# Kernel optimization log

Hardware: AMD Instinct MI355X
Metric: run time of the kernel (lower is better)

Reference implementation:

```python
import jax, jax.numpy as jnp
import numpy as np

N_QUBITS = 8
DEPTH = 2
INPUT_DIM = 128
HIDDEN = 128
SEQ = 128
BATCH = 512
DIM = 2 ** N_QUBITS

# Z expectation signs: wire 0 is the most-significant qubit of the state index.
_bits = (np.arange(DIM)[None, :] >> (N_QUBITS - 1 - np.arange(N_QUBITS)[:, None])) & 1
Z_SIGNS = jnp.asarray(1.0 - 2.0 * _bits, dtype=jnp.float32)  # [n_wires, DIM]


def _apply_1q(state, mat, wire):
    """Apply a 2x2 gate on `wire`. mat: [2,2] or batched [bsz,2,2]."""
    bsz = state.shape[0]
    st = state.reshape(bsz, 2 ** wire, 2, -1)
    if mat.ndim == 3:
        out = jnp.einsum('bij,bxjy->bxiy', mat, st)
    else:
        out = jnp.einsum('ij,bxjy->bxiy', mat, st)
    return out.reshape(bsz, DIM)


def _rx_mat(theta):  # theta: [bsz] -> [bsz,2,2] complex
    c = jnp.cos(theta * 0.5).astype(jnp.complex64)
    s = ((-1j) * jnp.sin(theta * 0.5)).astype(jnp.complex64)
    return jnp.stack([jnp.stack([c, s], -1), jnp.stack([s, c], -1)], -2)


def _ry_mat(theta):  # scalar theta -> [2,2] complex
    c = jnp.cos(theta * 0.5)
    s = jnp.sin(theta * 0.5)
    return jnp.stack([jnp.stack([c, -s]), jnp.stack([s, c])]).astype(jnp.complex64)


def _cnot_adj(state, wire):
    """CNOT control=wire, target=wire+1 (adjacent wires)."""
    bsz = state.shape[0]
    st = state.reshape(bsz, 2 ** wire, 4, -1)
    st = st[:, :, jnp.array([0, 1, 3, 2]), :]  # |10>-><|11| swap
    return st.reshape(bsz, DIM)


def _qgate(q_in, params):
    """Variational circuit: RX encoding (first N_QUBITS features of q_in),
    DEPTH x (RY layer + CNOT chain), measure Z on each wire."""
    bsz = q_in.shape[0]
    state = jnp.zeros((bsz, DIM), jnp.complex64).at[:, 0].set(1.0)
    for w in range(N_QUBITS):
        state = _apply_1q(state, _rx_mat(q_in[:, w]), w)
    for d in range(DEPTH):
        for w in range(N_QUBITS):
            state = _apply_1q(state, _ry_mat(params[d, w]), w)
        for w in range(N_QUBITS - 1):
            state = _cnot_adj(state, w)
    probs = state.real ** 2 + state.imag ** 2  # [bsz, DIM]
    return probs @ Z_SIGNS.T  # [bsz, n_wires]


def setup_inputs() -> dict:
    key = jax.random.key(0)
    ks = jax.random.split(key, 16)
    d_in = INPUT_DIM + HIDDEN
    inv = 1.0 / jnp.sqrt(jnp.float32(d_in))
    invq = 1.0 / jnp.sqrt(jnp.float32(N_QUBITS))
    return {
        'inputs': jax.random.normal(ks[0], (SEQ, BATCH, INPUT_DIM), jnp.float32),
        'Wq': jax.random.normal(ks[1], (4 * N_QUBITS, d_in), jnp.float32) * inv,
        'bq': jnp.zeros((4 * N_QUBITS,), jnp.float32),
        'pf': jax.random.normal(ks[2], (DEPTH, N_QUBITS), jnp.float32),
        'pi': jax.random.normal(ks[3], (DEPTH, N_QUBITS), jnp.float32),
        'pg': jax.random.normal(ks[4], (DEPTH, N_QUBITS), jnp.float32),
        'po': jax.random.normal(ks[5], (DEPTH, N_QUBITS), jnp.float32),
        'Wf': jax.random.normal(ks[6], (HIDDEN, N_QUBITS), jnp.float32) * invq,
        'bf': jnp.zeros((HIDDEN,), jnp.float32),
        'Wi': jax.random.normal(ks[7], (HIDDEN, N_QUBITS), jnp.float32) * invq,
        'bi': jnp.zeros((HIDDEN,), jnp.float32),
        'Wg': jax.random.normal(ks[8], (HIDDEN, N_QUBITS), jnp.float32) * invq,
        'bg': jnp.zeros((HIDDEN,), jnp.float32),
        'Wo': jax.random.normal(ks[9], (HIDDEN, N_QUBITS), jnp.float32) * invq,
        'bo': jnp.zeros((HIDDEN,), jnp.float32),
    }


def reference(inputs, Wq, bq, pf, pi, pg, po, Wf, bf, Wi, bi, Wg, bg, Wo, bo):
    bsz = inputs.shape[1]
    h0 = jnp.zeros((bsz, HIDDEN), jnp.float32)
    c0 = jnp.zeros((bsz, HIDDEN), jnp.float32)

    def step(carry, x):
        hx, cx = carry
        combined = jnp.concatenate([x, hx], axis=1)
        q_in = combined @ Wq.T + bq  # [bsz, 4*n_qubits]; only first n_qubits used per gate
        f = jax.nn.sigmoid(_qgate(q_in, pf) @ Wf.T + bf)
        i = jax.nn.sigmoid(_qgate(q_in, pi) @ Wi.T + bi)
        g = jnp.tanh(_qgate(q_in, pg) @ Wg.T + bg)
        o = jax.nn.sigmoid(_qgate(q_in, po) @ Wo.T + bo)
        cx_new = f * cx + i * g
        hx_new = o * jnp.tanh(cx_new)
        return (hx_new, cx_new), hx_new

    (hx, cx), outputs = jax.lax.scan(step, (h0, c0), inputs)
    return outputs, hx, cx
```

## Files before the change

### kernel.cpp

```cpp
#include <hip/hip_runtime.h>

#define SEQ 128
#define BATCH 512
#define IN_DIM 128
#define HID 128

typedef float vf2 __attribute__((ext_vector_type(2)));

#define LOG2E 1.4426950408889634f
#define INV2PI 0.15915494309189535f

__device__ __forceinline__ float rcp_f(float x) { return __builtin_amdgcn_rcpf(x); }
__device__ __forceinline__ float exp2_f(float x) { float r; asm("v_exp_f32 %0, %1" : "=v"(r) : "v"(x)); return r; }
__device__ __forceinline__ float sin2pi_f(float x) { float r; asm("v_sin_f32 %0, %1" : "=v"(r) : "v"(x)); return r; }
__device__ __forceinline__ float cos2pi_f(float x) { float r; asm("v_cos_f32 %0, %1" : "=v"(r) : "v"(x)); return r; }
__device__ __forceinline__ float tanh_f(float x) {
  return 1.0f - 2.0f * rcp_f(exp2_f(x * 2.885390082f) + 1.0f);
}

template <int CTRL>
__device__ __forceinline__ float dpp_add(float s) {
  return s + __int_as_float(__builtin_amdgcn_mov_dpp(__float_as_int(s), CTRL, 0xF, 0xF, true));
}
__device__ __forceinline__ float rdlane(float v, int src) {
  return __int_as_float(__builtin_amdgcn_readlane(__float_as_int(v), src));
}

__global__ __launch_bounds__(64) void qlstm_kernel(
    const float* __restrict__ X, const float* __restrict__ Wq, const float* __restrict__ bq,
    const float* __restrict__ pf, const float* __restrict__ pi_, const float* __restrict__ pg,
    const float* __restrict__ po, const float* __restrict__ Wf, const float* __restrict__ bf,
    const float* __restrict__ Wi, const float* __restrict__ bi, const float* __restrict__ Wg,
    const float* __restrict__ bg, const float* __restrict__ Wo, const float* __restrict__ bo,
    float* __restrict__ out)
{
  __shared__ __align__(16) float h_sh[HID];
  __shared__ __align__(16) float gsh[4 * HID];

  const int lane = threadIdx.x;
  const int r = lane >> 3, c = lane & 7;
  const int g = lane >> 4, p = lane & 15;
  const int b = blockIdx.x;

  const float* gW = (g == 0) ? Wf : (g == 1) ? Wi : (g == 2) ? Wg : Wo;
  const float* gB = (g == 0) ? bf : (g == 1) ? bi : (g == 2) ? bg : bo;
  const float* gP = (g == 0) ? pf : (g == 1) ? pi_ : (g == 2) ? pg : po;

  vf2 wx[8], wh[8];
  {
    const vf2* pxw = (const vf2*)(Wq + r * 256 + 16 * c);
    const vf2* phw = (const vf2*)(Wq + r * 256 + 128 + 16 * c);
#pragma unroll
    for (int j = 0; j < 8; ++j) { wx[j] = pxw[j]; wh[j] = phw[j]; }
  }
  const float bqv = bq[r];

  const float amul = (g == 2) ? 2.0f : 1.0f;
  const float oadd = (g == 2) ? -1.0f : 0.0f;
  const float ksc  = -amul * LOG2E;

  vf2 wg2[8][4];
#pragma unroll
  for (int w = 0; w < 8; ++w)
#pragma unroll
    for (int j = 0; j < 4; ++j) {
      wg2[w][j].x = gW[(8 * p + 2 * j)     * 8 + w] * ksc;
      wg2[w][j].y = gW[(8 * p + 2 * j + 1) * 8 + w] * ksc;
    }
  vf2 bias2[4];
#pragma unroll
  for (int j = 0; j < 4; ++j) {
    bias2[j].x = gB[8 * p + 2 * j]     * ksc;
    bias2[j].y = gB[8 * p + 2 * j + 1] * ksc;
  }
  vf2 cbsb[8]; float C1[8], S1[8];
#pragma unroll
  for (int w = 0; w < 8; ++w) {
    float th0 = gP[w], th1 = gP[8 + w];
    cbsb[w].x = cosf(th0); cbsb[w].y = sinf(th0);
    C1[w] = cosf(th1); S1[w] = sinf(th1);
  }

  vf2 c2; c2.x = 0.f; c2.y = 0.f;
  vf2 h2v; h2v.x = 0.f; h2v.y = 0.f;
  float4 hh0 = {0,0,0,0}, hh1 = {0,0,0,0}, hh2 = {0,0,0,0}, hh3 = {0,0,0,0};

  const float* xg = X + (size_t)b * IN_DIM + 16 * c;
  float* outp = out + (size_t)b * HID + 2 * lane;
  const float4* hp4 = (const float4*)(h_sh + 16 * c);

  float4 xP0, xP1, xP2, xP3, xQ0, xQ1, xQ2, xQ3;
  float xp_cur;
  {
    const float4* x0_ = (const float4*)xg;
    xP0 = x0_[0]; xP1 = x0_[1]; xP2 = x0_[2]; xP3 = x0_[3];
    vf2 ax = wx[0] * (vf2){xP0.x, xP0.y} + wx[1] * (vf2){xP0.z, xP0.w}
           + wx[2] * (vf2){xP1.x, xP1.y} + wx[3] * (vf2){xP1.z, xP1.w}
           + wx[4] * (vf2){xP2.x, xP2.y} + wx[5] * (vf2){xP2.z, xP2.w}
           + wx[6] * (vf2){xP3.x, xP3.y} + wx[7] * (vf2){xP3.z, xP3.w};
    xp_cur = ax.x + ax.y;
    const float4* x1_ = (const float4*)(xg + (size_t)(BATCH * IN_DIM));
    xQ0 = x1_[0]; xQ1 = x1_[1]; xQ2 = x1_[2]; xQ3 = x1_[3];
  }

#define QSTEP(U0, U1, U2, U3, L0, L1, L2, L3, T)                                      \
  {                                                                                   \
                      \
    vf2 aq = (vf2){xp_cur, 0.0f}                                                      \
           + wh[0] * (vf2){hh0.x, hh0.y} + wh[1] * (vf2){hh0.z, hh0.w}                \
           + wh[2] * (vf2){hh1.x, hh1.y} + wh[3] * (vf2){hh1.z, hh1.w}                \
           + wh[4] * (vf2){hh2.x, hh2.y} + wh[5] * (vf2){hh2.z, hh2.w}                \
           + wh[6] * (vf2){hh3.x, hh3.y} + wh[7] * (vf2){hh3.z, hh3.w};               \
    float s_ = aq.x + aq.y;                                                           \
    s_ = dpp_add<0xB1>(s_); s_ = dpp_add<0x4E>(s_); s_ = dpp_add<0x141>(s_);          \
    float z_ = s_ + bqv;                                                              \
    float m_ = z_ * INV2PI;                                                           \
    float sz_ = sin2pi_f(m_), cz_ = cos2pi_f(m_);                                     \
    float cqs[8], sqs[8];                                                             \
    _Pragma("unroll")                                                                 \
    for (int w = 0; w < 8; ++w) { cqs[w] = rdlane(cz_, 8 * w); sqs[w] = rdlane(sz_, 8 * w); } \
                                            \
    vf2 acc0 = bias2[0], acc1 = bias2[1], acc2 = bias2[2], acc3 = bias2[3];           \
    float u_, d_, P_, R_;                                                             \
    {                                                                                 \
      vf2 KA0 = cbsb[0] * cqs[0];                                                     \
      u_ = C1[0]; d_ = C1[0] * KA0.x;                                                 \
      P_ = -S1[0] * KA0.y; R_ = -S1[0] * sqs[0];                                      \
    }                                                                                 \
    _Pragma("unroll")                                                                 \
    for (int w = 1; w < 8; ++w) {                                                     \
      vf2 KA = cbsb[w] * cqs[w];                                                      \
      float K_ = KA.x, A2_ = KA.y, B2_ = sqs[w];                                      \
      float Md = fmaf(A2_, P_, d_);                                                   \
      float MP = fmaf(A2_, d_, P_);                                                   \
      float Mu = fmaf(K_, u_, -(B2_ * R_));                                           \
      float MR = fmaf(B2_, u_, K_ * R_);                                              \
      acc0 += Md * wg2[w - 1][0]; acc1 += Md * wg2[w - 1][1];                         \
      acc2 += Md * wg2[w - 1][2]; acc3 += Md * wg2[w - 1][3];                         \
      u_ = C1[w] * Md; d_ = C1[w] * Mu;                                               \
      P_ = -S1[w] * MP; R_ = -S1[w] * MR;                                             \
    }                                                                                 \
    float ev7_ = d_ + P_;                                                             \
    acc0 += ev7_ * wg2[7][0]; acc1 += ev7_ * wg2[7][1];                               \
    acc2 += ev7_ * wg2[7][2]; acc3 += ev7_ * wg2[7][3];                               \
                     \
    float av_[8] = {acc0.x, acc0.y, acc1.x, acc1.y, acc2.x, acc2.y, acc3.x, acc3.y};  \
    float o8[8];                                                                      \
    _Pragma("unroll")                                                                 \
    for (int k = 0; k < 8; ++k) {                                                     \
      float e_ = exp2_f(av_[k]);                                                      \
      o8[k] = fmaf(rcp_f(1.0f + e_), amul, oadd);                                     \
    }                                                                                 \
    {                                                                                 \
      float4* gp4 = (float4*)(gsh + g * HID + 8 * p);                                 \
      float4 w0; w0.x = o8[0]; w0.y = o8[1]; w0.z = o8[2]; w0.w = o8[3];              \
      float4 w1; w1.x = o8[4]; w1.y = o8[5]; w1.z = o8[6]; w1.w = o8[7];              \
      gp4[0] = w0; gp4[1] = w1;                                                       \
    }                                                                                 \
                          \
    {                                                                                 \
      vf2 axn = wx[0] * (vf2){U0.x, U0.y} + wx[1] * (vf2){U0.z, U0.w}                 \
              + wx[2] * (vf2){U1.x, U1.y} + wx[3] * (vf2){U1.z, U1.w}                 \
              + wx[4] * (vf2){U2.x, U2.y} + wx[5] * (vf2){U2.z, U2.w}                 \
              + wx[6] * (vf2){U3.x, U3.y} + wx[7] * (vf2){U3.z, U3.w};                \
      xp_cur = axn.x + axn.y;                                                         \
      int tl_ = ((T) + 2 < SEQ) ? (T) + 2 : (SEQ - 1);                                \
      const float4* xn_ = (const float4*)(xg + (size_t)tl_ * (BATCH * IN_DIM));       \
      L0 = xn_[0]; L1 = xn_[1]; L2 = xn_[2]; L3 = xn_[3];                             \
    }                                                                                 \
                                   \
    vf2 fv = *(const vf2*)(gsh + 0 * HID + 2 * lane);                                 \
    vf2 iv = *(const vf2*)(gsh + 1 * HID + 2 * lane);                                 \
    vf2 gv = *(const vf2*)(gsh + 2 * HID + 2 * lane);                                 \
    vf2 ov = *(const vf2*)(gsh + 3 * HID + 2 * lane);                                 \
    c2 = fv * c2 + iv * gv;                                                           \
    h2v.x = ov.x * tanh_f(c2.x);                                                      \
    h2v.y = ov.y * tanh_f(c2.y);                                                      \
    *(vf2*)(h_sh + 2 * lane) = h2v;                                                   \
                       \
    hh0 = hp4[0]; hh1 = hp4[1]; hh2 = hp4[2]; hh3 = hp4[3];                           \
    *(vf2*)(outp + (size_t)(T) * (BATCH * HID)) = h2v;                                \
  }

#pragma unroll 1
  for (int tt = 0; tt < SEQ; tt += 2) {
    QSTEP(xQ0, xQ1, xQ2, xQ3, xP0, xP1, xP2, xP3, tt);
    QSTEP(xP0, xP1, xP2, xP3, xQ0, xQ1, xQ2, xQ3, tt + 1);
  }
#undef QSTEP

  {
    size_t base = (size_t)SEQ * BATCH * HID;
    *(vf2*)(out + base + (size_t)b * HID + 2 * lane) = h2v;
    *(vf2*)(out + base + (size_t)BATCH * HID + (size_t)b * HID + 2 * lane) = c2;
  }
}

extern "C" void kernel_launch(void* const* d_in, const int* in_sizes, int n_in,
                              void* d_out, int out_size, void* d_ws, size_t ws_size,
                              hipStream_t stream) {
  (void)in_sizes; (void)n_in; (void)out_size; (void)d_ws; (void)ws_size;
  const float* X   = (const float*)d_in[0];
  const float* Wq  = (const float*)d_in[1];
  const float* bq  = (const float*)d_in[2];
  const float* pf  = (const float*)d_in[3];
  const float* pi_ = (const float*)d_in[4];
  const float* pg  = (const float*)d_in[5];
  const float* po  = (const float*)d_in[6];
  const float* Wf  = (const float*)d_in[7];
  const float* bf  = (const float*)d_in[8];
  const float* Wi  = (const float*)d_in[9];
  const float* bi  = (const float*)d_in[10];
  const float* Wg  = (const float*)d_in[11];
  const float* bg  = (const float*)d_in[12];
  const float* Wo  = (const float*)d_in[13];
  const float* bo  = (const float*)d_in[14];
  float* out = (float*)d_out;

  qlstm_kernel<<<BATCH, 64, 0, stream>>>(X, Wq, bq, pf, pi_, pg, po,
                                         Wf, bf, Wi, bi, Wg, bg, Wo, bo, out);
}
```

Before: 193.1 us.

## Process two batch rows per wavefront to interleave independent recurrent chains

Each 64-lane block now handles two batch elements at once. Their per-step dependency chains are interleaved to expose instruction-level parallelism and hide latency in the serial recurrence. The INV2PI scale is folded into the Wq weights and bias so the per-step multiply goes away. The x prefetch distance changes from two steps to one. The trade-off is half as many blocks (256 instead of 512 on a large GPU) and more registers per thread, which could lower occupancy or leave CUs idle.

```diff
diff --git a/kernel.cpp b/kernel.cpp
--- a/kernel.cpp
+++ b/kernel.cpp
@@ -4,6 +4,7 @@
 #define BATCH 512
 #define IN_DIM 128
 #define HID 128
+#define NCH 2
 
 typedef float vf2 __attribute__((ext_vector_type(2)));
 
@@ -34,13 +35,13 @@
     const float* __restrict__ bg, const float* __restrict__ Wo, const float* __restrict__ bo,
     float* __restrict__ out)
 {
-  __shared__ __align__(16) float h_sh[HID];
-  __shared__ __align__(16) float gsh[4 * HID];
+  __shared__ __align__(16) float gsh[NCH][4 * HID];
+  __shared__ __align__(16) float h_sh[NCH][HID];
 
   const int lane = threadIdx.x;
   const int r = lane >> 3, c = lane & 7;
   const int g = lane >> 4, p = lane & 15;
-  const int b = blockIdx.x;
+  const int b0 = blockIdx.x * NCH;
 
   const float* gW = (g == 0) ? Wf : (g == 1) ? Wi : (g == 2) ? Wg : Wo;
   const float* gB = (g == 0) ? bf : (g == 1) ? bi : (g == 2) ? bg : bo;
@@ -51,9 +52,9 @@
     const vf2* pxw = (const vf2*)(Wq + r * 256 + 16 * c);
     const vf2* phw = (const vf2*)(Wq + r * 256 + 128 + 16 * c);
 #pragma unroll
-    for (int j = 0; j < 8; ++j) { wx[j] = pxw[j]; wh[j] = phw[j]; }
-  }
-  const float bqv = bq[r];
+    for (int j = 0; j < 8; ++j) { wx[j] = pxw[j] * INV2PI; wh[j] = phw[j] * INV2PI; }
+  }
+  const float bqv = bq[r] * INV2PI;
 
   const float amul = (g == 2) ? 2.0f : 1.0f;
   const float oadd = (g == 2) ? -1.0f : 0.0f;
@@ -81,118 +82,151 @@
     C1[w] = cosf(th1); S1[w] = sinf(th1);
   }
 
-  vf2 c2; c2.x = 0.f; c2.y = 0.f;
-  vf2 h2v; h2v.x = 0.f; h2v.y = 0.f;
-  float4 hh0 = {0,0,0,0}, hh1 = {0,0,0,0}, hh2 = {0,0,0,0}, hh3 = {0,0,0,0};
-
-  const float* xg = X + (size_t)b * IN_DIM + 16 * c;
-  float* outp = out + (size_t)b * HID + 2 * lane;
-  const float4* hp4 = (const float4*)(h_sh + 16 * c);
-
-  float4 xP0, xP1, xP2, xP3, xQ0, xQ1, xQ2, xQ3;
-  float xp_cur;
-  {
-    const float4* x0_ = (const float4*)xg;
-    xP0 = x0_[0]; xP1 = x0_[1]; xP2 = x0_[2]; xP3 = x0_[3];
-    vf2 ax = wx[0] * (vf2){xP0.x, xP0.y} + wx[1] * (vf2){xP0.z, xP0.w}
-           + wx[2] * (vf2){xP1.x, xP1.y} + wx[3] * (vf2){xP1.z, xP1.w}
-           + wx[4] * (vf2){xP2.x, xP2.y} + wx[5] * (vf2){xP2.z, xP2.w}
-           + wx[6] * (vf2){xP3.x, xP3.y} + wx[7] * (vf2){xP3.z, xP3.w};
-    xp_cur = ax.x + ax.y;
-    const float4* x1_ = (const float4*)(xg + (size_t)(BATCH * IN_DIM));
-    xQ0 = x1_[0]; xQ1 = x1_[1]; xQ2 = x1_[2]; xQ3 = x1_[3];
-  }
-
-#define QSTEP(U0, U1, U2, U3, L0, L1, L2, L3, T)                                      \
-  {                                                                                   \
-                      \
-    vf2 aq = (vf2){xp_cur, 0.0f}                                                      \
-           + wh[0] * (vf2){hh0.x, hh0.y} + wh[1] * (vf2){hh0.z, hh0.w}                \
-           + wh[2] * (vf2){hh1.x, hh1.y} + wh[3] * (vf2){hh1.z, hh1.w}                \
-           + wh[4] * (vf2){hh2.x, hh2.y} + wh[5] * (vf2){hh2.z, hh2.w}                \
-           + wh[6] * (vf2){hh3.x, hh3.y} + wh[7] * (vf2){hh3.z, hh3.w};               \
-    float s_ = aq.x + aq.y;                                                           \
-    s_ = dpp_add<0xB1>(s_); s_ = dpp_add<0x4E>(s_); s_ = dpp_add<0x141>(s_);          \
-    float z_ = s_ + bqv;                                                              \
-    float m_ = z_ * INV2PI;                                                           \
-    float sz_ = sin2pi_f(m_), cz_ = cos2pi_f(m_);                                     \
-    float cqs[8], sqs[8];                                                             \
-    _Pragma("unroll")                                                                 \
-    for (int w = 0; w < 8; ++w) { cqs[w] = rdlane(cz_, 8 * w); sqs[w] = rdlane(sz_, 8 * w); } \
-                                            \
-    vf2 acc0 = bias2[0], acc1 = bias2[1], acc2 = bias2[2], acc3 = bias2[3];           \
-    float u_, d_, P_, R_;                                                             \
-    {                                                                                 \
-      vf2 KA0 = cbsb[0] * cqs[0];                                                     \
-      u_ = C1[0]; d_ = C1[0] * KA0.x;                                                 \
-      P_ = -S1[0] * KA0.y; R_ = -S1[0] * sqs[0];                                      \
-    }                                                                                 \
-    _Pragma("unroll")                                                                 \
-    for (int w = 1; w < 8; ++w) {                                                     \
-      vf2 KA = cbsb[w] * cqs[w];                                                      \
-      float K_ = KA.x, A2_ = KA.y, B2_ = sqs[w];                                      \
-      float Md = fmaf(A2_, P_, d_);                                                   \
-      float MP = fmaf(A2_, d_, P_);                                                   \
-      float Mu = fmaf(K_, u_, -(B2_ * R_));                                           \
-      float MR = fmaf(B2_, u_, K_ * R_);                                              \
-      acc0 += Md * wg2[w - 1][0]; acc1 += Md * wg2[w - 1][1];                         \
-      acc2 += Md * wg2[w - 1][2]; acc3 += Md * wg2[w - 1][3];                         \
-      u_ = C1[w] * Md; d_ = C1[w] * Mu;                                               \
-      P_ = -S1[w] * MP; R_ = -S1[w] * MR;                                             \
-    }                                                                                 \
-    float ev7_ = d_ + P_;                                                             \
-    acc0 += ev7_ * wg2[7][0]; acc1 += ev7_ * wg2[7][1];                               \
-    acc2 += ev7_ * wg2[7][2]; acc3 += ev7_ * wg2[7][3];                               \
-                     \
-    float av_[8] = {acc0.x, acc0.y, acc1.x, acc1.y, acc2.x, acc2.y, acc3.x, acc3.y};  \
-    float o8[8];                                                                      \
-    _Pragma("unroll")                                                                 \
-    for (int k = 0; k < 8; ++k) {                                                     \
-      float e_ = exp2_f(av_[k]);                                                      \
-      o8[k] = fmaf(rcp_f(1.0f + e_), amul, oadd);                                     \
-    }                                                                                 \
-    {                                                                                 \
-      float4* gp4 = (float4*)(gsh + g * HID + 8 * p);                                 \
-      float4 w0; w0.x = o8[0]; w0.y = o8[1]; w0.z = o8[2]; w0.w = o8[3];              \
-      float4 w1; w1.x = o8[4]; w1.y = o8[5]; w1.z = o8[6]; w1.w = o8[7];              \
-      gp4[0] = w0; gp4[1] = w1;                                                       \
-    }                                                                                 \
-                          \
-    {                                                                                 \
-      vf2 axn = wx[0] * (vf2){U0.x, U0.y} + wx[1] * (vf2){U0.z, U0.w}                 \
-              + wx[2] * (vf2){U1.x, U1.y} + wx[3] * (vf2){U1.z, U1.w}                 \
-              + wx[4] * (vf2){U2.x, U2.y} + wx[5] * (vf2){U2.z, U2.w}                 \
-              + wx[6] * (vf2){U3.x, U3.y} + wx[7] * (vf2){U3.z, U3.w};                \
-      xp_cur = axn.x + axn.y;                                                         \
-      int tl_ = ((T) + 2 < SEQ) ? (T) + 2 : (SEQ - 1);                                \
-      const float4* xn_ = (const float4*)(xg + (size_t)tl_ * (BATCH * IN_DIM));       \
-      L0 = xn_[0]; L1 = xn_[1]; L2 = xn_[2]; L3 = xn_[3];                             \
-    }                                                                                 \
-                                   \
-    vf2 fv = *(const vf2*)(gsh + 0 * HID + 2 * lane);                                 \
-    vf2 iv = *(const vf2*)(gsh + 1 * HID + 2 * lane);                                 \
-    vf2 gv = *(const vf2*)(gsh + 2 * HID + 2 * lane);                                 \
-    vf2 ov = *(const vf2*)(gsh + 3 * HID + 2 * lane);                                 \
-    c2 = fv * c2 + iv * gv;                                                           \
-    h2v.x = ov.x * tanh_f(c2.x);                                                      \
-    h2v.y = ov.y * tanh_f(c2.y);                                                      \
-    *(vf2*)(h_sh + 2 * lane) = h2v;                                                   \
-                       \
-    hh0 = hp4[0]; hh1 = hp4[1]; hh2 = hp4[2]; hh3 = hp4[3];                           \
-    *(vf2*)(outp + (size_t)(T) * (BATCH * HID)) = h2v;                                \
+  vf2 c2[NCH], h2v[NCH];
+  float4 hh[NCH][4];
+  float xp_cur[NCH];
+  const float* xg[NCH];
+  float* outp[NCH];
+#pragma unroll
+  for (int e = 0; e < NCH; ++e) {
+    c2[e].x = 0.f; c2[e].y = 0.f;
+    h2v[e].x = 0.f; h2v[e].y = 0.f;
+#pragma unroll
+    for (int j = 0; j < 4; ++j) { hh[e][j].x = 0.f; hh[e][j].y = 0.f; hh[e][j].z = 0.f; hh[e][j].w = 0.f; }
+    xg[e]   = X   + (size_t)(b0 + e) * IN_DIM + 16 * c;
+    outp[e] = out + (size_t)(b0 + e) * HID + 2 * lane;
+    const float4* x0_ = (const float4*)xg[e];
+    float4 a0 = x0_[0], a1 = x0_[1], a2 = x0_[2], a3 = x0_[3];
+    vf2 ax = wx[0] * (vf2){a0.x, a0.y} + wx[1] * (vf2){a0.z, a0.w}
+           + wx[2] * (vf2){a1.x, a1.y} + wx[3] * (vf2){a1.z, a1.w}
+           + wx[4] * (vf2){a2.x, a2.y} + wx[5] * (vf2){a2.z, a2.w}
+           + wx[6] * (vf2){a3.x, a3.y} + wx[7] * (vf2){a3.z, a3.w};
+    xp_cur[e] = ax.x + ax.y;
   }
 
 #pragma unroll 1
-  for (int tt = 0; tt < SEQ; tt += 2) {
-    QSTEP(xQ0, xQ1, xQ2, xQ3, xP0, xP1, xP2, xP3, tt);
-    QSTEP(xP0, xP1, xP2, xP3, xQ0, xQ1, xQ2, xQ3, tt + 1);
-  }
-#undef QSTEP
+  for (int t = 0; t < SEQ; ++t) {
+    float zz[NCH];
+#pragma unroll
+    for (int e = 0; e < NCH; ++e) {
+      vf2 aq = (vf2){xp_cur[e], 0.0f}
+             + wh[0] * (vf2){hh[e][0].x, hh[e][0].y} + wh[1] * (vf2){hh[e][0].z, hh[e][0].w}
+             + wh[2] * (vf2){hh[e][1].x, hh[e][1].y} + wh[3] * (vf2){hh[e][1].z, hh[e][1].w}
+             + wh[4] * (vf2){hh[e][2].x, hh[e][2].y} + wh[5] * (vf2){hh[e][2].z, hh[e][2].w}
+             + wh[6] * (vf2){hh[e][3].x, hh[e][3].y} + wh[7] * (vf2){hh[e][3].z, hh[e][3].w};
+      float s_ = aq.x + aq.y;
+      s_ = dpp_add<0xB1>(s_); s_ = dpp_add<0x4E>(s_); s_ = dpp_add<0x141>(s_);
+      zz[e] = s_ + bqv;
+    }
+    float szv[NCH], czv[NCH];
+#pragma unroll
+    for (int e = 0; e < NCH; ++e) { szv[e] = sin2pi_f(zz[e]); czv[e] = cos2pi_f(zz[e]); }
+
+    float4 xl[NCH][4];
+    {
+      const int tn = (t + 1 < SEQ) ? t + 1 : SEQ - 1;
+#pragma unroll
+      for (int e = 0; e < NCH; ++e) {
+        const float4* xn_ = (const float4*)(xg[e] + (size_t)tn * (BATCH * IN_DIM));
+#pragma unroll
+        for (int j = 0; j < 4; ++j) xl[e][j] = xn_[j];
+      }
+    }
+
+    float cqs[NCH][8], sqs[NCH][8];
+#pragma unroll
+    for (int e = 0; e < NCH; ++e)
+#pragma unroll
+      for (int w = 0; w < 8; ++w) {
+        cqs[e][w] = rdlane(czv[e], 8 * w);
+        sqs[e][w] = rdlane(szv[e], 8 * w);
+      }
+
+    vf2 acc[NCH][4];
+    float u_[NCH], d_[NCH], P_[NCH], R_[NCH];
+#pragma unroll
+    for (int e = 0; e < NCH; ++e) {
+      acc[e][0] = bias2[0]; acc[e][1] = bias2[1]; acc[e][2] = bias2[2]; acc[e][3] = bias2[3];
+      vf2 KA0 = cbsb[0] * cqs[e][0];
+      u_[e] = C1[0]; d_[e] = C1[0] * KA0.x;
+      P_[e] = -S1[0] * KA0.y; R_[e] = -S1[0] * sqs[e][0];
+    }
+#pragma unroll
+    for (int w = 1; w < 8; ++w) {
+#pragma unroll
+      for (int e = 0; e < NCH; ++e) {
+        vf2 KA = cbsb[w] * cqs[e][w];
+        float K_ = KA.x, A2_ = KA.y, B2_ = sqs[e][w];
+        float Md = fmaf(A2_, P_[e], d_[e]);
+        float MP = fmaf(A2_, d_[e], P_[e]);
+        float Mu = fmaf(K_, u_[e], -(B2_ * R_[e]));
+        float MR = fmaf(B2_, u_[e], K_ * R_[e]);
+        acc[e][0] += Md * wg2[w - 1][0]; acc[e][1] += Md * wg2[w - 1][1];
+        acc[e][2] += Md * wg2[w - 1][2]; acc[e][3] += Md * wg2[w - 1][3];
+        u_[e] = C1[w] * Md; d_[e] = C1[w] * Mu;
+        P_[e] = -S1[w] * MP; R_[e] = -S1[w] * MR;
+      }
+    }
+#pragma unroll
+    for (int e = 0; e < NCH; ++e) {
+      float ev7_ = d_[e] + P_[e];
+      acc[e][0] += ev7_ * wg2[7][0]; acc[e][1] += ev7_ * wg2[7][1];
+      acc[e][2] += ev7_ * wg2[7][2]; acc[e][3] += ev7_ * wg2[7][3];
+    }
+
+#pragma unroll
+    for (int e = 0; e < NCH; ++e) {
+      float av_[8] = {acc[e][0].x, acc[e][0].y, acc[e][1].x, acc[e][1].y,
+                      acc[e][2].x, acc[e][2].y, acc[e][3].x, acc[e][3].y};
+      float o8[8];
+#pragma unroll
+      for (int k = 0; k < 8; ++k) {
+        float ex_ = exp2_f(av_[k]);
+        o8[k] = fmaf(rcp_f(1.0f + ex_), amul, oadd);
+      }
+      float4* gp4 = (float4*)(&gsh[e][g * HID + 8 * p]);
+      float4 w0; w0.x = o8[0]; w0.y = o8[1]; w0.z = o8[2]; w0.w = o8[3];
+      float4 w1; w1.x = o8[4]; w1.y = o8[5]; w1.z = o8[6]; w1.w = o8[7];
+      gp4[0] = w0; gp4[1] = w1;
+    }
+
+#pragma unroll
+    for (int e = 0; e < NCH; ++e) {
+      vf2 fv = *(const vf2*)(&gsh[e][0 * HID + 2 * lane]);
+      vf2 iv = *(const vf2*)(&gsh[e][1 * HID + 2 * lane]);
+      vf2 gv = *(const vf2*)(&gsh[e][2 * HID + 2 * lane]);
+      vf2 ov = *(const vf2*)(&gsh[e][3 * HID + 2 * lane]);
+      c2[e] = fv * c2[e] + iv * gv;
+      h2v[e].x = ov.x * tanh_f(c2[e].x);
+      h2v[e].y = ov.y * tanh_f(c2[e].y);
+      *(vf2*)(&h_sh[e][2 * lane]) = h2v[e];
+    }
+#pragma unroll
+    for (int e = 0; e < NCH; ++e) {
+      const float4* hp4 = (const float4*)(&h_sh[e][16 * c]);
+      hh[e][0] = hp4[0]; hh[e][1] = hp4[1]; hh[e][2] = hp4[2]; hh[e][3] = hp4[3];
+    }
+#pragma unroll
+    for (int e = 0; e < NCH; ++e)
+      *(vf2*)(outp[e] + (size_t)t * (BATCH * HID)) = h2v[e];
+
+#pragma unroll
+    for (int e = 0; e < NCH; ++e) {
+      vf2 axn = wx[0] * (vf2){xl[e][0].x, xl[e][0].y} + wx[1] * (vf2){xl[e][0].z, xl[e][0].w}
+              + wx[2] * (vf2){xl[e][1].x, xl[e][1].y} + wx[3] * (vf2){xl[e][1].z, xl[e][1].w}
+              + wx[4] * (vf2){xl[e][2].x, xl[e][2].y} + wx[5] * (vf2){xl[e][2].z, xl[e][2].w}
+              + wx[6] * (vf2){xl[e][3].x, xl[e][3].y} + wx[7] * (vf2){xl[e][3].z, xl[e][3].w};
+      xp_cur[e] = axn.x + axn.y;
+    }
+  }
 
   {
     size_t base = (size_t)SEQ * BATCH * HID;
-    *(vf2*)(out + base + (size_t)b * HID + 2 * lane) = h2v;
-    *(vf2*)(out + base + (size_t)BATCH * HID + (size_t)b * HID + 2 * lane) = c2;
+#pragma unroll
+    for (int e = 0; e < NCH; ++e) {
+      *(vf2*)(out + base + (size_t)(b0 + e) * HID + 2 * lane) = h2v[e];
+      *(vf2*)(out + base + (size_t)BATCH * HID + (size_t)(b0 + e) * HID + 2 * lane) = c2[e];
+    }
   }
 }
 
@@ -217,6 +251,6 @@
   const float* bo  = (const float*)d_in[14];
   float* out = (float*)d_out;
 
-  qlstm_kernel<<<BATCH, 64, 0, stream>>>(X, Wq, bq, pf, pi_, pg, po,
-                                         Wf, bf, Wi, bi, Wg, bg, Wo, bo, out);
-}
+  qlstm_kernel<<<BATCH / NCH, 64, 0, stream>>>(X, Wq, bq, pf, pi_, pg, po,
+                                               Wf, bf, Wi, bi, Wg, bg, Wo, bo, out);
+}
```

Measured after the change: 217.5 us. 1.13x slower.

## Exchange gate activations via cross-lane permutes instead of LDS round-trip

Applied to the files above, without the earlier changes.

Removes the shared-memory gate buffer. Each lane now gathers its f/i/g/o gate values with permlane32/permlane16 swaps, or a ds_swizzle fallback, followed by selects, and the hidden-unit ownership is remapped so each lane owns units 8p+2g. It also folds the 1/(2π) scale into Wq and bq, balances the dot-product reduction trees, and replaces the two-step unrolled double-buffered x prefetch with a one-step-ahead prefetch. The goal is to cut LDS write/read latency on the serial recurrence critical path, at the cost of more permute and select instructions and a shorter prefetch distance.

```diff
diff --git a/kernel.cpp b/kernel.cpp
--- a/kernel.cpp
+++ b/kernel.cpp
@@ -24,6 +24,25 @@
 }
 __device__ __forceinline__ float rdlane(float v, int src) {
   return __int_as_float(__builtin_amdgcn_readlane(__float_as_int(v), src));
+}
+
+__device__ __forceinline__ void quarter_bcast(float x, float& r0, float& r1, float& r2, float& r3) {
+  unsigned xu = __float_as_uint(x);
+  auto pr = __builtin_amdgcn_permlane32_swap(xu, xu, false, false);
+#if __has_builtin(__builtin_amdgcn_permlane16_swap)
+  auto lo = __builtin_amdgcn_permlane16_swap(pr[0], pr[0], false, false);
+  auto hi = __builtin_amdgcn_permlane16_swap(pr[1], pr[1], false, false);
+  r0 = __uint_as_float(lo[0]); r1 = __uint_as_float(lo[1]);
+  r2 = __uint_as_float(hi[0]); r3 = __uint_as_float(hi[1]);
+#else
+  unsigned s0 = (unsigned)__builtin_amdgcn_ds_swizzle((int)pr[0], 0x401F);
+  unsigned s1 = (unsigned)__builtin_amdgcn_ds_swizzle((int)pr[1], 0x401F);
+  const bool qo = (threadIdx.x >> 4) & 1;
+  r0 = __uint_as_float(qo ? s0 : pr[0]);
+  r1 = __uint_as_float(qo ? pr[0] : s0);
+  r2 = __uint_as_float(qo ? s1 : pr[1]);
+  r3 = __uint_as_float(qo ? pr[1] : s1);
+#endif
 }
 
 __global__ __launch_bounds__(64) void qlstm_kernel(
@@ -35,12 +54,14 @@
     float* __restrict__ out)
 {
   __shared__ __align__(16) float h_sh[HID];
-  __shared__ __align__(16) float gsh[4 * HID];
 
   const int lane = threadIdx.x;
   const int r = lane >> 3, c = lane & 7;
   const int g = lane >> 4, p = lane & 15;
   const int b = blockIdx.x;
+  const int D0 = 8 * p + 2 * g;
+  const bool gsel1 = (g & 1);
+  const bool gsel2 = (g >= 2);
 
   const float* gW = (g == 0) ? Wf : (g == 1) ? Wi : (g == 2) ? Wg : Wo;
   const float* gB = (g == 0) ? bf : (g == 1) ? bi : (g == 2) ? bg : bo;
@@ -51,9 +72,9 @@
     const vf2* pxw = (const vf2*)(Wq + r * 256 + 16 * c);
     const vf2* phw = (const vf2*)(Wq + r * 256 + 128 + 16 * c);
 #pragma unroll
-    for (int j = 0; j < 8; ++j) { wx[j] = pxw[j]; wh[j] = phw[j]; }
-  }
-  const float bqv = bq[r];
+    for (int j = 0; j < 8; ++j) { wx[j] = pxw[j] * INV2PI; wh[j] = phw[j] * INV2PI; }
+  }
+  const float bqv = bq[r] * INV2PI;
 
   const float amul = (g == 2) ? 2.0f : 1.0f;
   const float oadd = (g == 2) ? -1.0f : 0.0f;
@@ -86,113 +107,123 @@
   float4 hh0 = {0,0,0,0}, hh1 = {0,0,0,0}, hh2 = {0,0,0,0}, hh3 = {0,0,0,0};
 
   const float* xg = X + (size_t)b * IN_DIM + 16 * c;
-  float* outp = out + (size_t)b * HID + 2 * lane;
+  float* outp = out + (size_t)b * HID + D0;
   const float4* hp4 = (const float4*)(h_sh + 16 * c);
 
-  float4 xP0, xP1, xP2, xP3, xQ0, xQ1, xQ2, xQ3;
   float xp_cur;
   {
     const float4* x0_ = (const float4*)xg;
-    xP0 = x0_[0]; xP1 = x0_[1]; xP2 = x0_[2]; xP3 = x0_[3];
-    vf2 ax = wx[0] * (vf2){xP0.x, xP0.y} + wx[1] * (vf2){xP0.z, xP0.w}
-           + wx[2] * (vf2){xP1.x, xP1.y} + wx[3] * (vf2){xP1.z, xP1.w}
-           + wx[4] * (vf2){xP2.x, xP2.y} + wx[5] * (vf2){xP2.z, xP2.w}
-           + wx[6] * (vf2){xP3.x, xP3.y} + wx[7] * (vf2){xP3.z, xP3.w};
+    float4 a0 = x0_[0], a1 = x0_[1], a2 = x0_[2], a3 = x0_[3];
+    vf2 t0 = wx[0] * (vf2){a0.x, a0.y} + wx[1] * (vf2){a0.z, a0.w};
+    vf2 t1 = wx[2] * (vf2){a1.x, a1.y} + wx[3] * (vf2){a1.z, a1.w};
+    vf2 t2 = wx[4] * (vf2){a2.x, a2.y} + wx[5] * (vf2){a2.z, a2.w};
+    vf2 t3 = wx[6] * (vf2){a3.x, a3.y} + wx[7] * (vf2){a3.z, a3.w};
+    vf2 ax = (t0 + t1) + (t2 + t3);
     xp_cur = ax.x + ax.y;
-    const float4* x1_ = (const float4*)(xg + (size_t)(BATCH * IN_DIM));
-    xQ0 = x1_[0]; xQ1 = x1_[1]; xQ2 = x1_[2]; xQ3 = x1_[3];
-  }
-
-#define QSTEP(U0, U1, U2, U3, L0, L1, L2, L3, T)                                      \
-  {                                                                                   \
-                      \
-    vf2 aq = (vf2){xp_cur, 0.0f}                                                      \
-           + wh[0] * (vf2){hh0.x, hh0.y} + wh[1] * (vf2){hh0.z, hh0.w}                \
-           + wh[2] * (vf2){hh1.x, hh1.y} + wh[3] * (vf2){hh1.z, hh1.w}                \
-           + wh[4] * (vf2){hh2.x, hh2.y} + wh[5] * (vf2){hh2.z, hh2.w}                \
-           + wh[6] * (vf2){hh3.x, hh3.y} + wh[7] * (vf2){hh3.z, hh3.w};               \
-    float s_ = aq.x + aq.y;                                                           \
-    s_ = dpp_add<0xB1>(s_); s_ = dpp_add<0x4E>(s_); s_ = dpp_add<0x141>(s_);          \
-    float z_ = s_ + bqv;                                                              \
-    float m_ = z_ * INV2PI;                                                           \
-    float sz_ = sin2pi_f(m_), cz_ = cos2pi_f(m_);                                     \
-    float cqs[8], sqs[8];                                                             \
-    _Pragma("unroll")                                                                 \
-    for (int w = 0; w < 8; ++w) { cqs[w] = rdlane(cz_, 8 * w); sqs[w] = rdlane(sz_, 8 * w); } \
-                                            \
-    vf2 acc0 = bias2[0], acc1 = bias2[1], acc2 = bias2[2], acc3 = bias2[3];           \
-    float u_, d_, P_, R_;                                                             \
-    {                                                                                 \
-      vf2 KA0 = cbsb[0] * cqs[0];                                                     \
-      u_ = C1[0]; d_ = C1[0] * KA0.x;                                                 \
-      P_ = -S1[0] * KA0.y; R_ = -S1[0] * sqs[0];                                      \
-    }                                                                                 \
-    _Pragma("unroll")                                                                 \
-    for (int w = 1; w < 8; ++w) {                                                     \
-      vf2 KA = cbsb[w] * cqs[w];                                                      \
-      float K_ = KA.x, A2_ = KA.y, B2_ = sqs[w];                                      \
-      float Md = fmaf(A2_, P_, d_);                                                   \
-      float MP = fmaf(A2_, d_, P_);                                                   \
-      float Mu = fmaf(K_, u_, -(B2_ * R_));                                           \
-      float MR = fmaf(B2_, u_, K_ * R_);                                              \
-      acc0 += Md * wg2[w - 1][0]; acc1 += Md * wg2[w - 1][1];                         \
-      acc2 += Md * wg2[w - 1][2]; acc3 += Md * wg2[w - 1][3];                         \
-      u_ = C1[w] * Md; d_ = C1[w] * Mu;                                               \
-      P_ = -S1[w] * MP; R_ = -S1[w] * MR;                                             \
-    }                                                                                 \
-    float ev7_ = d_ + P_;                                                             \
-    acc0 += ev7_ * wg2[7][0]; acc1 += ev7_ * wg2[7][1];                               \
-    acc2 += ev7_ * wg2[7][2]; acc3 += ev7_ * wg2[7][3];                               \
-                     \
-    float av_[8] = {acc0.x, acc0.y, acc1.x, acc1.y, acc2.x, acc2.y, acc3.x, acc3.y};  \
-    float o8[8];                                                                      \
-    _Pragma("unroll")                                                                 \
-    for (int k = 0; k < 8; ++k) {                                                     \
-      float e_ = exp2_f(av_[k]);                                                      \
-      o8[k] = fmaf(rcp_f(1.0f + e_), amul, oadd);                                     \
-    }                                                                                 \
-    {                                                                                 \
-      float4* gp4 = (float4*)(gsh + g * HID + 8 * p);                                 \
-      float4 w0; w0.x = o8[0]; w0.y = o8[1]; w0.z = o8[2]; w0.w = o8[3];              \
-      float4 w1; w1.x = o8[4]; w1.y = o8[5]; w1.z = o8[6]; w1.w = o8[7];              \
-      gp4[0] = w0; gp4[1] = w1;                                                       \
-    }                                                                                 \
-                          \
-    {                                                                                 \
-      vf2 axn = wx[0] * (vf2){U0.x, U0.y} + wx[1] * (vf2){U0.z, U0.w}                 \
-              + wx[2] * (vf2){U1.x, U1.y} + wx[3] * (vf2){U1.z, U1.w}                 \
-              + wx[4] * (vf2){U2.x, U2.y} + wx[5] * (vf2){U2.z, U2.w}                 \
-              + wx[6] * (vf2){U3.x, U3.y} + wx[7] * (vf2){U3.z, U3.w};                \
-      xp_cur = axn.x + axn.y;                                                         \
-      int tl_ = ((T) + 2 < SEQ) ? (T) + 2 : (SEQ - 1);                                \
-      const float4* xn_ = (const float4*)(xg + (size_t)tl_ * (BATCH * IN_DIM));       \
-      L0 = xn_[0]; L1 = xn_[1]; L2 = xn_[2]; L3 = xn_[3];                             \
-    }                                                                                 \
-                                   \
-    vf2 fv = *(const vf2*)(gsh + 0 * HID + 2 * lane);                                 \
-    vf2 iv = *(const vf2*)(gsh + 1 * HID + 2 * lane);                                 \
-    vf2 gv = *(const vf2*)(gsh + 2 * HID + 2 * lane);                                 \
-    vf2 ov = *(const vf2*)(gsh + 3 * HID + 2 * lane);                                 \
-    c2 = fv * c2 + iv * gv;                                                           \
-    h2v.x = ov.x * tanh_f(c2.x);                                                      \
-    h2v.y = ov.y * tanh_f(c2.y);                                                      \
-    *(vf2*)(h_sh + 2 * lane) = h2v;                                                   \
-                       \
-    hh0 = hp4[0]; hh1 = hp4[1]; hh2 = hp4[2]; hh3 = hp4[3];                           \
-    *(vf2*)(outp + (size_t)(T) * (BATCH * HID)) = h2v;                                \
   }
 
 #pragma unroll 1
-  for (int tt = 0; tt < SEQ; tt += 2) {
-    QSTEP(xQ0, xQ1, xQ2, xQ3, xP0, xP1, xP2, xP3, tt);
-    QSTEP(xP0, xP1, xP2, xP3, xQ0, xQ1, xQ2, xQ3, tt + 1);
-  }
-#undef QSTEP
+  for (int t = 0; t < SEQ; ++t) {
+    float4 xl0, xl1, xl2, xl3;
+    {
+      const int tn = (t + 1 < SEQ) ? t + 1 : SEQ - 1;
+      const float4* xn_ = (const float4*)(xg + (size_t)tn * (BATCH * IN_DIM));
+      xl0 = xn_[0]; xl1 = xn_[1]; xl2 = xn_[2]; xl3 = xn_[3];
+    }
+
+    float zz;
+    {
+      vf2 t0 = wh[0] * (vf2){hh0.x, hh0.y} + wh[1] * (vf2){hh0.z, hh0.w};
+      vf2 t1 = wh[2] * (vf2){hh1.x, hh1.y} + wh[3] * (vf2){hh1.z, hh1.w};
+      vf2 t2 = wh[4] * (vf2){hh2.x, hh2.y} + wh[5] * (vf2){hh2.z, hh2.w};
+      vf2 t3 = wh[6] * (vf2){hh3.x, hh3.y} + wh[7] * (vf2){hh3.z, hh3.w};
+      vf2 aq = ((t0 + t1) + (t2 + t3)) + (vf2){xp_cur, 0.0f};
+      float s_ = aq.x + aq.y;
+      s_ = dpp_add<0xB1>(s_); s_ = dpp_add<0x4E>(s_); s_ = dpp_add<0x141>(s_);
+      zz = s_ + bqv;
+    }
+    float szv = sin2pi_f(zz), czv = cos2pi_f(zz);
+
+    float cqs[8], sqs[8];
+#pragma unroll
+    for (int w = 0; w < 8; ++w) { cqs[w] = rdlane(czv, 8 * w); sqs[w] = rdlane(szv, 8 * w); }
+
+    vf2 acc0 = bias2[0], acc1 = bias2[1], acc2 = bias2[2], acc3 = bias2[3];
+    float u_, d_, P_, R_;
+    {
+      vf2 KA0 = cbsb[0] * cqs[0];
+      u_ = C1[0]; d_ = C1[0] * KA0.x;
+      P_ = -S1[0] * KA0.y; R_ = -S1[0] * sqs[0];
+    }
+#pragma unroll
+    for (int w = 1; w < 8; ++w) {
+      vf2 KA = cbsb[w] * cqs[w];
+      float K_ = KA.x, A2_ = KA.y, B2_ = sqs[w];
+      float Md = fmaf(A2_, P_, d_);
+      float MP = fmaf(A2_, d_, P_);
+      float Mu = fmaf(K_, u_, -(B2_ * R_));
+      float MR = fmaf(B2_, u_, K_ * R_);
+      acc0 += Md * wg2[w - 1][0]; acc1 += Md * wg2[w - 1][1];
+      acc2 += Md * wg2[w - 1][2]; acc3 += Md * wg2[w - 1][3];
+      u_ = C1[w] * Md; d_ = C1[w] * Mu;
+      P_ = -S1[w] * MP; R_ = -S1[w] * MR;
+    }
+    float ev7_ = d_ + P_;
+    acc0 += ev7_ * wg2[7][0]; acc1 += ev7_ * wg2[7][1];
+    acc2 += ev7_ * wg2[7][2]; acc3 += ev7_ * wg2[7][3];
+
+    float av_[8] = {acc0.x, acc0.y, acc1.x, acc1.y, acc2.x, acc2.y, acc3.x, acc3.y};
+    float o8[8];
+#pragma unroll
+    for (int k = 0; k < 8; ++k) {
+      float e_ = exp2_f(av_[k]);
+      o8[k] = fmaf(rcp_f(1.0f + e_), amul, oadd);
+    }
+
+    float rE[4][4], rO[4][4];
+#pragma unroll
+    for (int j = 0; j < 4; ++j) {
+      quarter_bcast(o8[2 * j],     rE[j][0], rE[j][1], rE[j][2], rE[j][3]);
+      quarter_bcast(o8[2 * j + 1], rO[j][0], rO[j][1], rO[j][2], rO[j][3]);
+    }
+    vf2 fv, iv, gv, ov;
+    {
+      float lo, hi;
+#define SEL4(A0, A1, A2, A3, DST) \
+      lo = gsel1 ? (A1) : (A0); hi = gsel1 ? (A3) : (A2); DST = gsel2 ? hi : lo;
+      SEL4(rE[0][0], rE[1][0], rE[2][0], rE[3][0], fv.x)
+      SEL4(rO[0][0], rO[1][0], rO[2][0], rO[3][0], fv.y)
+      SEL4(rE[0][1], rE[1][1], rE[2][1], rE[3][1], iv.x)
+      SEL4(rO[0][1], rO[1][1], rO[2][1], rO[3][1], iv.y)
+      SEL4(rE[0][2], rE[1][2], rE[2][2], rE[3][2], gv.x)
+      SEL4(rO[0][2], rO[1][2], rO[2][2], rO[3][2], gv.y)
+      SEL4(rE[0][3], rE[1][3], rE[2][3], rE[3][3], ov.x)
+      SEL4(rO[0][3], rO[1][3], rO[2][3], rO[3][3], ov.y)
+#undef SEL4
+    }
+
+    c2 = fv * c2 + iv * gv;
+    h2v.x = ov.x * tanh_f(c2.x);
+    h2v.y = ov.y * tanh_f(c2.y);
+
+    *(vf2*)(h_sh + D0) = h2v;
+    hh0 = hp4[0]; hh1 = hp4[1]; hh2 = hp4[2]; hh3 = hp4[3];
+
+    {
+      vf2 t0 = wx[0] * (vf2){xl0.x, xl0.y} + wx[1] * (vf2){xl0.z, xl0.w};
+      vf2 t1 = wx[2] * (vf2){xl1.x, xl1.y} + wx[3] * (vf2){xl1.z, xl1.w};
+      vf2 t2 = wx[4] * (vf2){xl2.x, xl2.y} + wx[5] * (vf2){xl2.z, xl2.w};
+      vf2 t3 = wx[6] * (vf2){xl3.x, xl3.y} + wx[7] * (vf2){xl3.z, xl3.w};
+      vf2 axn = (t0 + t1) + (t2 + t3);
+      xp_cur = axn.x + axn.y;
+    }
+    *(vf2*)(outp + (size_t)t * (BATCH * HID)) = h2v;
+  }
 
   {
     size_t base = (size_t)SEQ * BATCH * HID;
-    *(vf2*)(out + base + (size_t)b * HID + 2 * lane) = h2v;
-    *(vf2*)(out + base + (size_t)BATCH * HID + (size_t)b * HID + 2 * lane) = c2;
+    *(vf2*)(out + base + (size_t)b * HID + D0) = h2v;
+    *(vf2*)(out + base + (size_t)BATCH * HID + (size_t)b * HID + D0) = c2;
   }
 }
 
```

Measured after the change: 214.6 us. 11.2% more time.
